# Kernel optimization log

Hardware: AMD Instinct MI355X
Metric: run time of the kernel (lower is better)

The kernel has to match this reference:

```python
import jax, jax.numpy as jnp
import numpy as np

B = 32
WH, WW = 24, 24
M = WH * WW          # 576 patch tokens
N = M + 1            # +1 cls token -> 577
DIM = 768
NH = 12
HD = DIM // NH       # 64
MLP_DIM = 3072
NRD = (2 * WH - 1) * (2 * WW - 1) + 3  # 2212 relative-distance entries
EPS = 1e-6
SCALE = HD ** (-0.5)


def _rel_index():
    # faithful reproduction of the torch buffer construction
    coords = np.stack(np.meshgrid(np.arange(WH), np.arange(WW), indexing='ij'))  # [2,WH,WW]
    flat = coords.reshape(2, -1)                                   # [2,M]
    rel = (flat[:, :, None] - flat[:, None, :]).transpose(1, 2, 0).astype(np.int64)  # [M,M,2]
    rel[..., 0] += WH - 1
    rel[..., 1] += WW - 1
    rel[..., 0] *= 2 * WW - 1
    idx = np.zeros((N, N), np.int64)
    idx[1:, 1:] = rel.sum(-1)
    idx[0, :] = NRD - 3
    idx[:, 0] = NRD - 2
    idx[0, 0] = NRD - 1
    return jnp.asarray(idx, jnp.int32)


def setup_inputs() -> dict:
    key = jax.random.key(0)
    ks = jax.random.split(key, 8)
    s = 0.02
    return {
        'x': jax.random.normal(ks[0], (B, N, DIM), jnp.float32),
        'norm1_g': jnp.ones((DIM,), jnp.float32),
        'norm1_b': jnp.zeros((DIM,), jnp.float32),
        'qkv_w': jax.random.normal(ks[1], (3 * DIM, DIM), jnp.float32) * s,
        'q_bias': jnp.zeros((DIM,), jnp.float32),
        'v_bias': jnp.zeros((DIM,), jnp.float32),
        'rpb_table': jax.random.normal(ks[2], (NRD, NH), jnp.float32) * s,
        'proj_w': jax.random.normal(ks[3], (DIM, DIM), jnp.float32) * s,
        'proj_b': jnp.zeros((DIM,), jnp.float32),
        'norm2_g': jnp.ones((DIM,), jnp.float32),
        'norm2_b': jnp.zeros((DIM,), jnp.float32),
        'fc1_w': jax.random.normal(ks[4], (MLP_DIM, DIM), jnp.float32) * s,
        'fc1_b': jnp.zeros((MLP_DIM,), jnp.float32),
        'fc2_w': jax.random.normal(ks[5], (DIM, MLP_DIM), jnp.float32) * s,
        'fc2_b': jnp.zeros((DIM,), jnp.float32),
        'rel_index': _rel_index(),
    }


def _ln(h, g, b):
    m = jnp.mean(h, -1, keepdims=True)
    v = jnp.mean(jnp.square(h - m), -1, keepdims=True)
    return (h - m) * jax.lax.rsqrt(v + EPS) * g + b


def reference(x, norm1_g, norm1_b, qkv_w, q_bias, v_bias, rpb_table, proj_w, proj_b,
              norm2_g, norm2_b, fc1_w, fc1_b, fc2_w, fc2_b, rel_index):
    Bq, Nq, _ = x.shape
    # --- attention branch ---
    h = _ln(x, norm1_g, norm1_b)
    qkv_bias = jnp.concatenate([q_bias, jnp.zeros_like(v_bias), v_bias])
    qkv = h @ qkv_w.T + qkv_bias                                # [B,N,3C]
    qkv = qkv.reshape(Bq, Nq, 3, NH, HD)
    q, k, v = qkv[:, :, 0], qkv[:, :, 1], qkv[:, :, 2]          # [B,N,H,D]
    attn = jnp.einsum('bnhd,bmhd->bhnm', q * SCALE, k)          # [B,H,N,N]
    rpb = rpb_table[rel_index]                                  # [N,N,H] gather
    attn = attn + jnp.transpose(rpb, (2, 0, 1))[None]           # [1,H,N,N]
    attn = jax.nn.softmax(attn, axis=-1)
    out = jnp.einsum('bhnm,bmhd->bnhd', attn, v).reshape(Bq, Nq, DIM)
    out = out @ proj_w.T + proj_b
    x = x + out
    # --- MLP branch ---
    h2 = _ln(x, norm2_g, norm2_b)
    m = jax.nn.gelu(h2 @ fc1_w.T + fc1_b, approximate=False)
    x = x + (m @ fc2_w.T + fc2_b)
    return x
```

## Files before the change

kernel.cpp:

```cpp
#include <hip/hip_runtime.h>
#include <hip/hip_bf16.h>
#include <math.h>

#define BATCH 32
#define NTOK 577
#define DIM 768
#define NHEAD 12
#define HDIM 64
#define MLP 3072
#define ROWS (BATCH*NTOK)
#define ATTN_SCALE 0.125f
#define LN_EPS 1e-6f
#define VST 584
#define RST 584
#define TK 64
#define NRT 145
#define SOFF 20.0f

typedef unsigned short u16;
typedef unsigned int u32;
typedef __attribute__((ext_vector_type(8))) short bf16x8;
typedef __attribute__((ext_vector_type(4))) float f32x4;

__device__ inline u16 f2bf(float f){
  u32 u = __float_as_uint(f);
  u32 r = (u + 0x7fffu + ((u>>16)&1u)) >> 16;
  return (u16)r;
}
__device__ inline float bf2f(u16 v){
  u32 u = ((u32)v)<<16; return __uint_as_float(u);
}

__device__ __forceinline__ void gload16(const u16* g, u16* l){
  __builtin_amdgcn_global_load_lds((const __attribute__((address_space(1))) void*)g,
                                   (__attribute__((address_space(3))) void*)l, 16, 0, 0);
}

__device__ inline float gelu_f(float v){
  float xa = fabsf(v)*0.70710678118654752f;
  float t = 1.0f/(1.0f + 0.3275911f*xa);
  float p = (((1.061405429f*t - 1.453152027f)*t + 1.421413741f)*t - 0.284496736f)*t + 0.254829592f;
  float erfv = 1.0f - p*t*__expf(-xa*xa);
  erfv = (v < 0.f) ? -erfv : erfv;
  return 0.5f*v*(1.0f + erfv);
}

__global__ void cvt4_kernel(const float* __restrict__ s0, int n0,
                            const float* __restrict__ s1, int n1,
                            const float* __restrict__ s2, int n2,
                            const float* __restrict__ s3, int n3,
                            u16* __restrict__ d0, u16* __restrict__ d1,
                            u16* __restrict__ d2, u16* __restrict__ d3){
  int i = blockIdx.x*256 + threadIdx.x;
  if(i < n0){ d0[i] = f2bf(s0[i]); return; }
  i -= n0;
  if(i < n1){ d1[i] = f2bf(s1[i]); return; }
  i -= n1;
  if(i < n2){ d2[i] = f2bf(s2[i]); return; }
  i -= n2;
  if(i < n3){ d3[i] = f2bf(s3[i]); }
}

__global__ void rpb_kernel(const int* __restrict__ rel, const float* __restrict__ table, u16* __restrict__ bias){
  int i = blockIdx.x*256 + threadIdx.x;
  const int nm = NTOK*NTOK;
  if(i >= NHEAD*nm) return;
  int h = i / nm;
  int r = i - h*nm;
  int n = r / NTOK, m = r - n*NTOK;
  bias[((size_t)h*NTOK + n)*RST + m] = f2bf(table[rel[r]*NHEAD + h]);
}

__global__ __launch_bounds__(256) void ln_kernel(const float* __restrict__ in, const float* __restrict__ g,
                                                 const float* __restrict__ b, u16* __restrict__ out){
  int row = blockIdx.x;
  const float* p = in + (size_t)row*DIM;
  int t = threadIdx.x;
  float v0 = p[t], v1 = p[t+256], v2 = p[t+512];
  float s = v0+v1+v2;
  #pragma unroll
  for(int off=32; off; off>>=1) s += __shfl_xor(s, off);
  __shared__ float red[8];
  int wv = t>>6;
  if((t&63)==0) red[wv] = s;
  __syncthreads();
  float mean = (red[0]+red[1]+red[2]+red[3]) * (1.0f/768.0f);
  float d0=v0-mean, d1=v1-mean, d2=v2-mean;
  float q = d0*d0 + d1*d1 + d2*d2;
  #pragma unroll
  for(int off=32; off; off>>=1) q += __shfl_xor(q, off);
  if((t&63)==0) red[4+wv] = q;
  __syncthreads();
  float var = (red[4]+red[5]+red[6]+red[7]) * (1.0f/768.0f);
  float inv = rsqrtf(var + LN_EPS);
  u16* po = out + (size_t)row*DIM;
  po[t]     = f2bf(d0*inv*g[t]     + b[t]);
  po[t+256] = f2bf(d1*inv*g[t+256] + b[t+256]);
  po[t+512] = f2bf(d2*inv*g[t+512] + b[t+512]);
}

template<int MODE, int NC>
__global__ __launch_bounds__(256) void gemm_kernel(
    const u16* __restrict__ A, const u16* __restrict__ Bt,
    int M, int K,
    const float* __restrict__ b0, const float* __restrict__ b1,
    const float* __restrict__ resid, float* __restrict__ outf,
    u16* __restrict__ o0, u16* __restrict__ o1, u16* __restrict__ o2)
{
  __shared__ __align__(16) u16 As[3][4096];
  __shared__ __align__(16) u16 Bs[3][4096];

  int id = blockIdx.x;
  int xcd = id & 7, sblk = id >> 3;
  int rg = sblk / NC, c = sblk - rg*NC;
  int r = xcd + 8*rg;
  if(r >= NRT) return;
  const int rowTile = r*128, colTile = c*128;

  const int tx = threadIdx.x;
  const int wave = tx>>6, lane = tx&63;
  const int wr = (wave>>1)*64, wc = (wave&1)*64;
  const int lrow = lane&15, kq = lane>>4, l7 = lane&7;

  const int sl  = (lane&7) ^ (lane>>3);
  const int hr  = sl>>2;
  const int c8  = (sl&3)*8;
  const int rstage = 16*wave + (lane>>3) + 64*hr;
  const u32 offA0 = (u32)min(rowTile + rstage,     M-1)*(u32)K + c8;
  const u32 offA1 = (u32)min(rowTile + rstage + 8, M-1)*(u32)K + c8;
  const u32 offB0 = (u32)(colTile + rstage)*(u32)K + c8;
  const u32 offB1 = offB0 + 8u*(u32)K;
  const int dst0 = (2*wave)*512, dst1 = dst0 + 512;

  int eA[4], eB[4];
  #pragma unroll
  for(int i=0;i<4;i++)
    eA[i] = (i*16 + lrow)*64 + (((kq + (wr>>4)) ^ l7)*8);
  #pragma unroll
  for(int j=0;j<4;j++)
    eB[j] = (j*16 + lrow)*64 + (((kq + (wc>>4)) ^ l7)*8);

  f32x4 acc[4][4];
  #pragma unroll
  for(int i=0;i<4;i++)
    #pragma unroll
    for(int j=0;j<4;j++){ f32x4 z = {0.f,0.f,0.f,0.f}; acc[i][j]=z; }

  #define STAGEH(BUF, KOFF) { \
    gload16(A  + (offA0 + (KOFF)), &As[BUF][dst0]); \
    gload16(A  + (offA1 + (KOFF)), &As[BUF][dst1]); \
    gload16(Bt + (offB0 + (KOFF)), &Bs[BUF][dst0]); \
    gload16(Bt + (offB1 + (KOFF)), &Bs[BUF][dst1]); \
  }

  #define COMPUTE(BUF) { \
    bf16x8 af_[4], bf_[4]; \
    _Pragma("unroll") \
    for(int i_=0;i_<4;i_++) af_[i_] = *(const bf16x8*)(&As[BUF][eA[i_]]); \
    _Pragma("unroll") \
    for(int j_=0;j_<4;j_++) bf_[j_] = *(const bf16x8*)(&Bs[BUF][eB[j_]]); \
    _Pragma("unroll") \
    for(int i_=0;i_<4;i_++) \
      _Pragma("unroll") \
      for(int j_=0;j_<4;j_++) \
        acc[i_][j_] = __builtin_amdgcn_mfma_f32_16x16x32_bf16(af_[i_], bf_[j_], acc[i_][j_], 0,0,0); \
  }

  #define PHASE(SLOT, U) { \
    if((U)+2 < NT){ \
      STAGEH(((SLOT)+2)%3, (u32)((U)+2)<<5); \
      asm volatile("s_waitcnt vmcnt(8)" ::: "memory"); \
    } else if((U)+1 < NT){ \
      asm volatile("s_waitcnt vmcnt(4)" ::: "memory"); \
    } else { \
      asm volatile("s_waitcnt vmcnt(0)" ::: "memory"); \
    } \
    __builtin_amdgcn_s_barrier(); \
    __builtin_amdgcn_sched_barrier(0); \
    COMPUTE(SLOT); \
    __builtin_amdgcn_s_barrier(); \
  }

  const int NT = K >> 5;
  STAGEH(0, 0u);
  STAGEH(1, 1u<<5);
  for(int t=0; t<NT; t+=3){
    PHASE(0, t);
    PHASE(1, t+1);
    PHASE(2, t+2);
  }
  #undef PHASE
  #undef STAGEH
  #undef COMPUTE

  #pragma unroll
  for(int i=0;i<4;i++){
    int rbase = rowTile + wr + i*16 + kq*4;
    #pragma unroll
    for(int j=0;j<4;j++){
      int col = colTile + wc + j*16 + lrow;
      #pragma unroll
      for(int rr=0; rr<4; rr++){
        int rrow = rbase + rr;
        if(rrow >= M) continue;
        float v = acc[i][j][rr];
        if(MODE==0){
          int part = col/DIM, cc = col - part*DIM;
          int head = cc>>6, d = cc&63;
          int bb = rrow/NTOK, n = rrow - bb*NTOK;
          size_t bh = (size_t)bb*NHEAD + head;
          if(part==0){ v = (v + b0[cc])*ATTN_SCALE; o0[(bh*NTOK + n)*HDIM + d] = f2bf(v); }
          else if(part==1){ o1[(bh*NTOK + n)*HDIM + d] = f2bf(v); }
          else { v += b1[cc]; o2[(bh*HDIM + d)*VST + n] = f2bf(v); }
        } else if(MODE==1){
          outf[(size_t)rrow*DIM + col] = v + b0[col] + resid[(size_t)rrow*DIM + col];
        } else if(MODE==2){
          o0[(size_t)rrow*MLP + col] = f2bf(gelu_f(v + b0[col]));
        } else {
          outf[(size_t)rrow*DIM + col] = v + b0[col] + resid[(size_t)rrow*DIM + col];
        }
      }
    }
  }
}

__global__ __launch_bounds__(256) void fattn_kernel(
    const u16* __restrict__ q, const u16* __restrict__ k, const u16* __restrict__ vt,
    const u16* __restrict__ rpb, u16* __restrict__ out)
{
  int bid = blockIdx.x;
  int qt = bid / 384;
  int rem = bid - qt*384;
  int h = rem >> 5, b = rem & 31;
  int bh = b*NHEAD + h;
  int r0 = qt*64;

  __shared__ __align__(16) u16 Ks[64][72];
  __shared__ __align__(16) u16 Vs[64][72];
  __shared__ __align__(16) u16 Rs[64][72];
  __shared__ __align__(16) u16 Pw[4][16][72];

  int tx = threadIdx.x, wave = tx>>6, lane = tx&63;
  int lcol = lane & 15;
  int quad = lane >> 4;
  int rw0 = r0 + wave*16;

  bf16x8 aq0 = {0,0,0,0,0,0,0,0}, aq1 = {0,0,0,0,0,0,0,0};
  {
    int qrow = rw0 + lcol;
    if(qrow < NTOK){
      const u16* qp = q + ((size_t)bh*NTOK + qrow)*HDIM + quad*8;
      aq0 = *(const bf16x8*)(qp);
      aq1 = *(const bf16x8*)(qp + 32);
    }
  }

  f32x4 o[4];
  #pragma unroll
  for(int j=0;j<4;j++){ f32x4 z={0.f,0.f,0.f,0.f}; o[j]=z; }
  float lpart[4] = {0.f,0.f,0.f,0.f};

  int sr = tx>>3, sc = (tx&7)*8;

  const u16* kbase = k  + (size_t)bh*NTOK*HDIM;
  const u16* vbase = vt + (size_t)bh*HDIM*VST;
  const u16* rbase = rpb + ((size_t)h*NTOK + r0)*RST;

  for(int kt=0; kt<10; kt++){
    int key0 = kt*TK;
    *(bf16x8*)(&Ks[sr][sc])    = *(const bf16x8*)(kbase + (size_t)(key0+sr)*HDIM + sc);
    *(bf16x8*)(&Ks[32+sr][sc]) = *(const bf16x8*)(kbase + (size_t)(key0+32+sr)*HDIM + sc);
    *(bf16x8*)(&Vs[sr][sc])    = *(const bf16x8*)(vbase + (size_t)sr*VST + key0 + sc);
    *(bf16x8*)(&Vs[32+sr][sc]) = *(const bf16x8*)(vbase + (size_t)(32+sr)*VST + key0 + sc);
    *(bf16x8*)(&Rs[sr][sc])    = *(const bf16x8*)(rbase + (size_t)sr*RST + key0 + sc);
    *(bf16x8*)(&Rs[32+sr][sc]) = *(const bf16x8*)(rbase + (size_t)(32+sr)*RST + key0 + sc);
    __syncthreads();

    f32x4 s[4];
    #pragma unroll
    for(int c=0;c<4;c++){
      f32x4 z = {0.f,0.f,0.f,0.f};
      bf16x8 kb0 = *(const bf16x8*)(&Ks[16*c+lcol][quad*8]);
      bf16x8 kb1 = *(const bf16x8*)(&Ks[16*c+lcol][32+quad*8]);
      z = __builtin_amdgcn_mfma_f32_16x16x32_bf16(aq0, kb0, z, 0,0,0);
      z = __builtin_amdgcn_mfma_f32_16x16x32_bf16(aq1, kb1, z, 0,0,0);
      s[c] = z;
    }

    #pragma unroll
    for(int rr=0; rr<4; rr++){
      int qloc = wave*16 + quad*4 + rr;
      #pragma unroll
      for(int c=0;c<4;c++){
        int key = key0 + 16*c + lcol;
        float sv = (key < NTOK) ? s[c][rr] + bf2f(Rs[qloc][16*c+lcol]) : -1e30f;
        float pe = __expf(sv - SOFF);
        lpart[rr] += pe;
        Pw[wave][quad*4+rr][16*c+lcol] = f2bf(pe);
      }
    }
    bf16x8 ap0 = *(const bf16x8*)(&Pw[wave][lcol][quad*8]);
    bf16x8 ap1 = *(const bf16x8*)(&Pw[wave][lcol][32+quad*8]);
    #pragma unroll
    for(int j=0;j<4;j++){
      bf16x8 vb0 = *(const bf16x8*)(&Vs[16*j+lcol][quad*8]);
      bf16x8 vb1 = *(const bf16x8*)(&Vs[16*j+lcol][32+quad*8]);
      o[j] = __builtin_amdgcn_mfma_f32_16x16x32_bf16(ap0, vb0, o[j], 0,0,0);
      o[j] = __builtin_amdgcn_mfma_f32_16x16x32_bf16(ap1, vb1, o[j], 0,0,0);
    }
    __syncthreads();
  }

  #pragma unroll
  for(int rr=0;rr<4;rr++){
    float ts = lpart[rr];
    ts += __shfl_xor(ts, 1);
    ts += __shfl_xor(ts, 2);
    ts += __shfl_xor(ts, 4);
    ts += __shfl_xor(ts, 8);
    lpart[rr] = ts;
  }
  #pragma unroll
  for(int rr=0;rr<4;rr++){
    int n = rw0 + quad*4 + rr;
    if(n >= NTOK) continue;
    float inv = 1.0f / lpart[rr];
    u16* op = out + ((size_t)b*NTOK + n)*DIM + h*HDIM;
    #pragma unroll
    for(int j=0;j<4;j++)
      op[16*j + lcol] = f2bf(o[j][rr]*inv);
  }
}

extern "C" void kernel_launch(void* const* d_in, const int* in_sizes, int n_in,
                              void* d_out, int out_size, void* d_ws, size_t ws_size,
                              hipStream_t stream)
{
  const float* x      = (const float*)d_in[0];
  const float* n1g    = (const float*)d_in[1];
  const float* n1b    = (const float*)d_in[2];
  const float* qkvw   = (const float*)d_in[3];
  const float* qbias  = (const float*)d_in[4];
  const float* vbias  = (const float*)d_in[5];
  const float* rpbt   = (const float*)d_in[6];
  const float* projw  = (const float*)d_in[7];
  const float* projb  = (const float*)d_in[8];
  const float* n2g    = (const float*)d_in[9];
  const float* n2b    = (const float*)d_in[10];
  const float* fc1w   = (const float*)d_in[11];
  const float* fc1b   = (const float*)d_in[12];
  const float* fc2w   = (const float*)d_in[13];
  const float* fc2b   = (const float*)d_in[14];
  const int*   relidx = (const int*)d_in[15];

  char* ws = (char*)d_ws;
  const size_t WQ_OFF  = 0;
  const size_t WP_OFF  = 3538944;
  const size_t W1_OFF  = 4718592;
  const size_t W2_OFF  = 9437184;
  const size_t RPB_OFF = 14155776;
  const size_t H_OFF   = 30136576;
  const size_t Q_OFF   = H_OFF + 28360704;
  const size_t K_OFF   = Q_OFF + 28360704;
  const size_t V_OFF   = K_OFF + 28360704;
  const size_t ATT_OFF = V_OFF + 28704896;
  const size_t X1_OFF  = ATT_OFF + 28360704;
  const size_t M_OFF   = H_OFF;
  const size_t H2_OFF  = ATT_OFF;

  u16* wq   = (u16*)(ws + WQ_OFF);
  u16* wp   = (u16*)(ws + WP_OFF);
  u16* w1   = (u16*)(ws + W1_OFF);
  u16* w2   = (u16*)(ws + W2_OFF);
  u16* rpbb = (u16*)(ws + RPB_OFF);
  u16* hb   = (u16*)(ws + H_OFF);
  u16* qbuf = (u16*)(ws + Q_OFF);
  u16* kbuf = (u16*)(ws + K_OFF);
  u16* vbuf = (u16*)(ws + V_OFF);
  u16* attb = (u16*)(ws + ATT_OFF);
  float* x1 = (float*)(ws + X1_OFF);
  u16* mbuf = (u16*)(ws + M_OFF);
  u16* h2   = (u16*)(ws + H2_OFF);
  float* outp = (float*)d_out;

  const int ncvt = 2304*768 + 768*768 + 3072*768 + 3072*768;
  cvt4_kernel<<<(ncvt+255)/256, 256, 0, stream>>>(qkvw, 2304*768, projw, 768*768,
                                                  fc1w, 3072*768, fc2w, 3072*768,
                                                  wq, wp, w1, w2);
  rpb_kernel<<<(NHEAD*NTOK*NTOK+255)/256, 256, 0, stream>>>(relidx, rpbt, rpbb);

  const int GRP = 8 * ((NRT + 7)/8);

  ln_kernel<<<ROWS, 256, 0, stream>>>(x, n1g, n1b, hb);
  gemm_kernel<0,18><<<GRP*18, 256, 0, stream>>>(hb, wq, ROWS, DIM, qbias, vbias,
                                                nullptr, nullptr, qbuf, kbuf, vbuf);
  fattn_kernel<<<10*384, 256, 0, stream>>>(qbuf, kbuf, vbuf, rpbb, attb);
  gemm_kernel<1,6><<<GRP*6, 256, 0, stream>>>(attb, wp, ROWS, DIM, projb, nullptr,
                                              x, x1, nullptr, nullptr, nullptr);
  ln_kernel<<<ROWS, 256, 0, stream>>>(x1, n2g, n2b, h2);
  gemm_kernel<2,24><<<GRP*24, 256, 0, stream>>>(h2, w1, ROWS, DIM, fc1b, nullptr,
                                                nullptr, nullptr, mbuf, nullptr, nullptr);
  gemm_kernel<3,6><<<GRP*6, 256, 0, stream>>>(mbuf, w2, ROWS, MLP, fc2b, nullptr,
                                              x1, outp, nullptr, nullptr, nullptr);
}
```

Measured before the change: 882.3 us.

## Widen GEMM tile to 128x256 with 8 waves and inline-asm LDS reads

The GEMM kernel moves from a 128x128 tile with 4 waves to a 128x256 tile with 8 waves (512 threads), so each A tile staged in LDS is reused across twice as many output columns and the number of column blocks is halved. Staging is redistributed so each thread issues one A load and two B loads per k-step, and the vmcnt waits are adjusted to match. LDS fragment reads become explicit ds_read_b128 with immediate offsets from precomputed per-stage pointers, followed by a single lgkmcnt wait. LDS use per block rises and there are fewer blocks per GEMM, which risks lower occupancy and worse tail utilisation for the smaller projection GEMMs.

```diff
diff --git a/kernel.cpp b/kernel.cpp
--- a/kernel.cpp
+++ b/kernel.cpp
@@ -21,6 +21,7 @@
 typedef unsigned int u32;
 typedef __attribute__((ext_vector_type(8))) short bf16x8;
 typedef __attribute__((ext_vector_type(4))) float f32x4;
+typedef const __attribute__((address_space(3))) u16* lds_cp;
 
 __device__ inline u16 f2bf(float f){
   u32 u = __float_as_uint(f);
@@ -100,7 +101,7 @@
 }
 
 template<int MODE, int NC>
-__global__ __launch_bounds__(256) void gemm_kernel(
+__global__ __launch_bounds__(512) void gemm_kernel(
     const u16* __restrict__ A, const u16* __restrict__ Bt,
     int M, int K,
     const float* __restrict__ b0, const float* __restrict__ b1,
@@ -108,57 +109,62 @@
     u16* __restrict__ o0, u16* __restrict__ o1, u16* __restrict__ o2)
 {
   __shared__ __align__(16) u16 As[3][4096];
-  __shared__ __align__(16) u16 Bs[3][4096];
+  __shared__ __align__(16) u16 Bs[3][8192];
 
   int id = blockIdx.x;
   int xcd = id & 7, sblk = id >> 3;
   int rg = sblk / NC, c = sblk - rg*NC;
   int r = xcd + 8*rg;
   if(r >= NRT) return;
-  const int rowTile = r*128, colTile = c*128;
+  const int rowTile = r*128, colTile = c*256;
 
   const int tx = threadIdx.x;
   const int wave = tx>>6, lane = tx&63;
-  const int wr = (wave>>1)*64, wc = (wave&1)*64;
+  const int wr = (wave>>2)*64;
+  const int wc = (wave&3)*64;
   const int lrow = lane&15, kq = lane>>4, l7 = lane&7;
 
   const int sl  = (lane&7) ^ (lane>>3);
   const int hr  = sl>>2;
   const int c8  = (sl&3)*8;
-  const int rstage = 16*wave + (lane>>3) + 64*hr;
-  const u32 offA0 = (u32)min(rowTile + rstage,     M-1)*(u32)K + c8;
-  const u32 offA1 = (u32)min(rowTile + rstage + 8, M-1)*(u32)K + c8;
-  const u32 offB0 = (u32)(colTile + rstage)*(u32)K + c8;
+  const int rowA = 8*wave + (lane>>3) + 64*hr;
+  const u32 offA = (u32)min(rowTile + rowA, M-1)*(u32)K + c8;
+  const int dstA = wave*512;
+  const int grp = wave>>2, w4 = wave&3;
+  const int rowB = grp*128 + 16*w4 + (lane>>3) + 64*hr;
+  const u32 offB0 = (u32)(colTile + rowB)*(u32)K + c8;
   const u32 offB1 = offB0 + 8u*(u32)K;
-  const int dst0 = (2*wave)*512, dst1 = dst0 + 512;
-
-  int eA[4], eB[4];
+  const int dstB0 = grp*4096 + (2*w4)*512, dstB1 = dstB0 + 512;
+
+  const int eA0 = lrow*64 + (((kq + (wr>>4)) ^ l7)*8);
+  const int eB0 = (wc>>7)*4096 + lrow*64 + (((kq + ((wc>>4)&4)) ^ l7)*8);
+  lds_cp pA0 = (lds_cp)&As[0][eA0], pA1 = (lds_cp)&As[1][eA0], pA2 = (lds_cp)&As[2][eA0];
+  lds_cp pB0 = (lds_cp)&Bs[0][eB0], pB1 = (lds_cp)&Bs[1][eB0], pB2 = (lds_cp)&Bs[2][eB0];
+
+  f32x4 acc[4][4];
   #pragma unroll
   for(int i=0;i<4;i++)
-    eA[i] = (i*16 + lrow)*64 + (((kq + (wr>>4)) ^ l7)*8);
-  #pragma unroll
-  for(int j=0;j<4;j++)
-    eB[j] = (j*16 + lrow)*64 + (((kq + (wc>>4)) ^ l7)*8);
-
-  f32x4 acc[4][4];
-  #pragma unroll
-  for(int i=0;i<4;i++)
     #pragma unroll
     for(int j=0;j<4;j++){ f32x4 z = {0.f,0.f,0.f,0.f}; acc[i][j]=z; }
 
-  #define STAGEH(BUF, KOFF) { \
-    gload16(A  + (offA0 + (KOFF)), &As[BUF][dst0]); \
-    gload16(A  + (offA1 + (KOFF)), &As[BUF][dst1]); \
-    gload16(Bt + (offB0 + (KOFF)), &Bs[BUF][dst0]); \
-    gload16(Bt + (offB1 + (KOFF)), &Bs[BUF][dst1]); \
-  }
-
-  #define COMPUTE(BUF) { \
+  #define STAGEH(S, KOFF) { \
+    gload16(A  + (offA  + (KOFF)), &As[S][dstA]); \
+    gload16(Bt + (offB0 + (KOFF)), &Bs[S][dstB0]); \
+    gload16(Bt + (offB1 + (KOFF)), &Bs[S][dstB1]); \
+  }
+
+  #define COMPUTE(PA, PB) { \
     bf16x8 af_[4], bf_[4]; \
-    _Pragma("unroll") \
-    for(int i_=0;i_<4;i_++) af_[i_] = *(const bf16x8*)(&As[BUF][eA[i_]]); \
-    _Pragma("unroll") \
-    for(int j_=0;j_<4;j_++) bf_[j_] = *(const bf16x8*)(&Bs[BUF][eB[j_]]); \
+    asm volatile("ds_read_b128 %0, %1"             : "=v"(af_[0]) : "v"(PA)); \
+    asm volatile("ds_read_b128 %0, %1 offset:2048" : "=v"(af_[1]) : "v"(PA)); \
+    asm volatile("ds_read_b128 %0, %1 offset:4096" : "=v"(af_[2]) : "v"(PA)); \
+    asm volatile("ds_read_b128 %0, %1 offset:6144" : "=v"(af_[3]) : "v"(PA)); \
+    asm volatile("ds_read_b128 %0, %1"             : "=v"(bf_[0]) : "v"(PB)); \
+    asm volatile("ds_read_b128 %0, %1 offset:2048" : "=v"(bf_[1]) : "v"(PB)); \
+    asm volatile("ds_read_b128 %0, %1 offset:4096" : "=v"(bf_[2]) : "v"(PB)); \
+    asm volatile("ds_read_b128 %0, %1 offset:6144" : "=v"(bf_[3]) : "v"(PB)); \
+    asm volatile("s_waitcnt lgkmcnt(0)" ::: "memory"); \
+    __builtin_amdgcn_sched_barrier(0); \
     _Pragma("unroll") \
     for(int i_=0;i_<4;i_++) \
       _Pragma("unroll") \
@@ -166,18 +172,17 @@
         acc[i_][j_] = __builtin_amdgcn_mfma_f32_16x16x32_bf16(af_[i_], bf_[j_], acc[i_][j_], 0,0,0); \
   }
 
-  #define PHASE(SLOT, U) { \
+  #define PHASE(S, PAx, PBx, U) { \
     if((U)+2 < NT){ \
-      STAGEH(((SLOT)+2)%3, (u32)((U)+2)<<5); \
-      asm volatile("s_waitcnt vmcnt(8)" ::: "memory"); \
+      STAGEH(((S)+2)%3, (u32)((U)+2)<<5); \
+      asm volatile("s_waitcnt vmcnt(6)" ::: "memory"); \
     } else if((U)+1 < NT){ \
-      asm volatile("s_waitcnt vmcnt(4)" ::: "memory"); \
+      asm volatile("s_waitcnt vmcnt(3)" ::: "memory"); \
     } else { \
       asm volatile("s_waitcnt vmcnt(0)" ::: "memory"); \
     } \
     __builtin_amdgcn_s_barrier(); \
-    __builtin_amdgcn_sched_barrier(0); \
-    COMPUTE(SLOT); \
+    COMPUTE(PAx, PBx); \
     __builtin_amdgcn_s_barrier(); \
   }
 
@@ -185,9 +190,9 @@
   STAGEH(0, 0u);
   STAGEH(1, 1u<<5);
   for(int t=0; t<NT; t+=3){
-    PHASE(0, t);
-    PHASE(1, t+1);
-    PHASE(2, t+2);
+    PHASE(0, pA0, pB0, t);
+    PHASE(1, pA1, pB1, t+1);
+    PHASE(2, pA2, pB2, t+2);
   }
   #undef PHASE
   #undef STAGEH
@@ -392,14 +397,14 @@
   const int GRP = 8 * ((NRT + 7)/8);
 
   ln_kernel<<<ROWS, 256, 0, stream>>>(x, n1g, n1b, hb);
-  gemm_kernel<0,18><<<GRP*18, 256, 0, stream>>>(hb, wq, ROWS, DIM, qbias, vbias,
-                                                nullptr, nullptr, qbuf, kbuf, vbuf);
+  gemm_kernel<0,9><<<GRP*9, 512, 0, stream>>>(hb, wq, ROWS, DIM, qbias, vbias,
+                                              nullptr, nullptr, qbuf, kbuf, vbuf);
   fattn_kernel<<<10*384, 256, 0, stream>>>(qbuf, kbuf, vbuf, rpbb, attb);
-  gemm_kernel<1,6><<<GRP*6, 256, 0, stream>>>(attb, wp, ROWS, DIM, projb, nullptr,
+  gemm_kernel<1,3><<<GRP*3, 512, 0, stream>>>(attb, wp, ROWS, DIM, projb, nullptr,
                                               x, x1, nullptr, nullptr, nullptr);
   ln_kernel<<<ROWS, 256, 0, stream>>>(x1, n2g, n2b, h2);
-  gemm_kernel<2,24><<<GRP*24, 256, 0, stream>>>(h2, w1, ROWS, DIM, fc1b, nullptr,
+  gemm_kernel<2,12><<<GRP*12, 512, 0, stream>>>(h2, w1, ROWS, DIM, fc1b, nullptr,
                                                 nullptr, nullptr, mbuf, nullptr, nullptr);
-  gemm_kernel<3,6><<<GRP*6, 256, 0, stream>>>(mbuf, w2, ROWS, MLP, fc2b, nullptr,
+  gemm_kernel<3,3><<<GRP*3, 512, 0, stream>>>(mbuf, w2, ROWS, MLP, fc2b, nullptr,
                                               x1, outp, nullptr, nullptr, nullptr);
 }
```

Result: faster. 764.2 us (-13.4%).
